# Kernel tuning notes

Measured on AMD Instinct MI355X. Metric: run time of the kernel, lower is better.

Reference implementation:

```python
import jax, jax.numpy as jnp
import numpy as np

N_ENT = 100000
N_USR = 30000
N_TOT = N_ENT + N_USR
N_REL = 32
D = 64
E = 500000
INTER = 500000
N_LAYERS = 2
SLOPE = 0.01  # torch nn.LeakyReLU default negative slope


def _seg_softmax(logits, seg, n):
    # sparse softmax over rows (segments)
    m = jax.ops.segment_max(logits, seg, num_segments=n)
    ex = jnp.exp(logits - m[seg])
    den = jax.ops.segment_sum(ex, seg, num_segments=n)
    return ex / den[seg]


def setup_inputs() -> dict:
    key = jax.random.key(0)
    k = jax.random.split(key, 14)
    all_embed = jax.random.normal(k[0], (N_TOT, D), jnp.float32) * 0.1
    rel_embed = jax.random.normal(k[1], (N_REL, D), jnp.float32) * 0.1
    Wk_w = jax.random.normal(k[2], (D, 2 * D), jnp.float32) / np.sqrt(2 * D)
    Wk_b = jnp.zeros((D,), jnp.float32)
    Wa_w = jax.random.normal(k[3], (D, D), jnp.float32) / np.sqrt(D)
    Wb_w = jax.random.normal(k[4], (D, D), jnp.float32) / np.sqrt(D)
    # KG edge lists (head entity, tail entity, relation)
    h_list = jnp.sort(jax.random.randint(k[5], (E,), 0, N_ENT))
    t_list = jax.random.randint(k[6], (E,), 0, N_ENT)
    r_list = jax.random.randint(k[7], (E,), 0, N_REL)
    # bipartite interaction matrix A_in (symmetric, items rows first then users)
    u = jax.random.randint(k[8], (INTER,), 0, N_USR)
    it = jax.random.randint(k[9], (INTER,), 0, N_ENT)
    a_row = jnp.concatenate([it, N_ENT + u])
    a_col = jnp.concatenate([N_ENT + u, it])
    a_vals = jax.random.uniform(k[10], (2 * INTER,), jnp.float32) * 0.01
    # calc_score ids: user ids are offset by n_entities in the concatenated table
    user_ids = N_ENT + jax.random.randint(k[11], (1024,), 0, N_USR)
    item_ids = jax.random.randint(k[12], (2048,), 0, N_ENT)
    return dict(all_embed=all_embed, rel_embed=rel_embed, Wk_w=Wk_w, Wk_b=Wk_b,
                Wa_w=Wa_w, Wb_w=Wb_w, a_vals=a_vals, user_ids=user_ids,
                item_ids=item_ids, h_list=h_list, t_list=t_list, r_list=r_list,
                a_row=a_row, a_col=a_col)


def _get_embeddings(all_embed, rel_embed, Wk_w, Wk_b, Wa_w, Wb_w, a_vals,
                    h_list, t_list, r_list, a_row, a_col):
    e_ent = all_embed[:N_ENT]
    e_usr = all_embed[N_ENT:]
    user_list = [e_usr]
    item_list = [e_ent]
    e_items_dual = e_ent
    e_users_curr = e_usr
    e_ent_curr = e_ent
    r_e = rel_embed[r_list]  # (E, D) -- constant across layers
    for _ in range(N_LAYERS):
        # --- KG attention (Eq. 2): gather + concat + linear + dot + leakyrelu ---
        h_e = e_ent_curr[h_list]            # (E, D)
        t_e = e_ent_curr[t_list]            # (E, D)
        cat = jnp.concatenate([t_e, h_e], axis=1)   # (E, 2D)
        trans = cat @ Wk_w.T + Wk_b                 # (E, D)
        logits = jnp.sum(trans * r_e, axis=1)       # (E,)
        vals = jnp.where(logits >= 0, logits, SLOPE * logits)
        alpha = _seg_softmax(vals, h_list, N_ENT)   # row-wise sparse softmax
        # --- KG aggregation (Eq. 1): spmm ---
        e_items_kg = jax.ops.segment_sum(alpha[:, None] * t_e, h_list,
                                         num_segments=N_ENT)
        # --- IG aggregation (Eq. 3 & 6): spmm with A_in ---
        ig_in = jnp.concatenate([e_items_dual, e_users_curr], axis=0)  # (N_TOT, D)
        ig_out = jax.ops.segment_sum(a_vals[:, None] * ig_in[a_col], a_row,
                                     num_segments=N_TOT)
        e_items_collab = ig_out[:N_ENT]
        e_users_new = ig_out[N_ENT:]
        # --- fusion gate (Eq. 4, 5) ---
        g = jax.nn.sigmoid(e_items_kg @ Wa_w.T + e_items_collab @ Wb_w.T)
        e_items_dual = g * e_items_kg + (1.0 - g) * e_items_collab
        item_list.append(e_items_collab)
        user_list.append(e_users_new)
        e_users_curr = e_users_new
        e_ent_curr = e_items_kg
    item_final = sum(item_list)
    user_final = sum(user_list)
    return jnp.concatenate([item_final, user_final], axis=0)


def reference(all_embed, rel_embed, Wk_w, Wk_b, Wa_w, Wb_w, a_vals,
              user_ids, item_ids, h_list, t_list, r_list, a_row, a_col):
    all_final = _get_embeddings(all_embed, rel_embed, Wk_w, Wk_b, Wa_w, Wb_w,
                                a_vals, h_list, t_list, r_list, a_row, a_col)
    user_e = all_final[user_ids]   # (Bu, D)
    item_e = all_final[item_ids]   # (Bi, D)
    return user_e @ item_e.T       # (Bu, Bi)
```

## Files before the change

### kernel.cpp

```cpp
#include <hip/hip_runtime.h>

#define N_ENT 100000
#define N_USR 30000
#define N_TOTN 130000
#define N_RELC 32
#define DIM 64
#define NEDGE 500000
#define INTER 500000
#define SLOPE 0.01f
#define CPT_NB 127
#define FILL_NB 489
#define MARK_NB 489
#define ATT_NB 512
#define SP_NB 512
#define RSTR 64
#define KGOFF_NB 1954

typedef unsigned char u8;
typedef unsigned long long u64;

__device__ __forceinline__ float grp_sum16(float v){
  v += __shfl_xor(v, 8, 64);
  v += __shfl_xor(v, 4, 64);
  v += __shfl_xor(v, 2, 64);
  v += __shfl_xor(v, 1, 64);
  return v;
}

__global__ void __launch_bounds__(256) k_prep(
    const float* __restrict__ rel, const float* __restrict__ Wk,
    const float* __restrict__ Wkb, float* __restrict__ m, float* __restrict__ b,
    const int* __restrict__ user_ids, const int* __restrict__ item_ids,
    u8* __restrict__ r2_item, u8* __restrict__ r2_user,
    const int* __restrict__ h_list, int* __restrict__ off){
  int bid = blockIdx.x;
  if (bid < 17){
    int idx = bid*256 + threadIdx.x;
    if (idx < N_RELC*128){
      int r = idx >> 7, j = idx & 127;
      float s = 0.f;
      for (int d = 0; d < DIM; ++d) s += rel[r*DIM+d] * Wk[d*128+j];
      m[idx] = s;
    } else if (idx < N_RELC*128 + N_RELC){
      int r = idx - N_RELC*128;
      float s = 0.f;
      for (int d = 0; d < DIM; ++d) s += Wkb[d] * rel[r*DIM+d];
      b[r] = s;
    }
  } else if (bid < 29){
    int i = (bid - 17)*256 + threadIdx.x;
    if (i < 1024) r2_user[user_ids[i] - N_ENT] = 1;
    else if (i < 3072) r2_item[item_ids[i - 1024]] = 1;
  } else {
    int e = (bid - 29)*256 + threadIdx.x;
    if (e <= NEDGE){
      int hc = (e < NEDGE) ? h_list[e] : N_ENT;
      int hp = (e == 0) ? -1 : h_list[e-1];
      for (int s = hp+1; s <= hc; ++s) off[s] = e;
    }
  }
}

__global__ void k_mark(const int4* __restrict__ a_row4, const int4* __restrict__ a_col4,
                       const u8* __restrict__ r2_item, const u8* __restrict__ r2_user,
                       u8* __restrict__ need_d, u8* __restrict__ need_u){
  int i = blockIdx.x*256 + threadIdx.x;
  if (i >= INTER/4) return;
  int4 ar = a_row4[i];
  int4 ac = a_col4[i];
  #pragma unroll
  for (int k = 0; k < 4; ++k){
    int it = (&ar.x)[k];
    int uu = (&ac.x)[k] - N_ENT;
    if (r2_item[it]) need_u[uu] = 1;
    if (r2_user[uu]) need_d[it] = 1;
  }
}

__global__ void __launch_bounds__(256) k_buildfill(
    const int* __restrict__ a_row, const int* __restrict__ a_col,
    const float* __restrict__ a_vals,
    const u8* __restrict__ need_d, const u8* __restrict__ need_u,
    const u8* __restrict__ r2_item, const u8* __restrict__ r2_user,
    int* __restrict__ list_gate, int* __restrict__ list_s1,
    int* __restrict__ counters, int* __restrict__ cnt, int2* __restrict__ csr){
  if (blockIdx.x < CPT_NB){
    __shared__ u64 mg_sh[16], ms_sh[16];
    __shared__ int pre_g[16], pre_s[16];
    __shared__ int base_sh[2];
    int t = threadIdx.x;
    int wave = t >> 6, lane = t & 63;
    bool pg[4], ps[4];
    int ibase = blockIdx.x*1024;
    #pragma unroll
    for (int k = 0; k < 4; ++k){
      int i = ibase + k*256 + t;
      bool g = false, s = false;
      if (i < N_TOTN){
        if (i < N_ENT){ g = need_d[i] != 0; s = (!g) && (r2_item[i] != 0); }
        else { int u = i - N_ENT; s = (need_u[u] != 0) || (r2_user[u] != 0); }
      }
      pg[k] = g; ps[k] = s;
      u64 mg = __ballot(g), ms = __ballot(s);
      if (lane == 0){ mg_sh[k*4 + wave] = mg; ms_sh[k*4 + wave] = ms; }
    }
    __syncthreads();
    if (t == 0){
      int sg = 0, ss = 0;
      for (int j = 0; j < 16; ++j){
        pre_g[j] = sg; sg += __popcll(mg_sh[j]);
        pre_s[j] = ss; ss += __popcll(ms_sh[j]);
      }
      base_sh[0] = sg ? atomicAdd(&counters[0], sg) : 0;
      base_sh[1] = ss ? atomicAdd(&counters[1], ss) : 0;
    }
    __syncthreads();
    int bg = base_sh[0], bs = base_sh[1];
    u64 lmask = (1ull << lane) - 1;
    #pragma unroll
    for (int k = 0; k < 4; ++k){
      int i = ibase + k*256 + t;
      if (pg[k]) list_gate[bg + pre_g[k*4+wave] + __popcll(mg_sh[k*4+wave] & lmask)] = i;
      if (ps[k]) list_s1 [bs + pre_s[k*4+wave] + __popcll(ms_sh[k*4+wave] & lmask)] = i;
    }
  } else {
    int i = (blockIdx.x - CPT_NB)*256 + threadIdx.x;
    if (i >= INTER/4) return;
    int4 ar = ((const int4*)a_row)[i];
    int4 ac = ((const int4*)a_col)[i];
    float4 av0 = ((const float4*)a_vals)[i];
    float4 av1 = ((const float4*)(a_vals + INTER))[i];
    #pragma unroll
    for (int k = 0; k < 4; ++k){
      int it = (&ar.x)[k];
      int uc = (&ac.x)[k];
      int uu = uc - N_ENT;
      if (need_d[it] | r2_item[it]){
        int p = atomicAdd(&cnt[it], 1);
        if (p < RSTR) csr[((size_t)it << 6) + p] = make_int2(uc, __float_as_int((&av0.x)[k]));
      }
      if (need_u[uu] | r2_user[uu]){
        int p = atomicAdd(&cnt[uc], 1);
        if (p < RSTR) csr[((size_t)uc << 6) + p] = make_int2(it, __float_as_int((&av1.x)[k]));
      }
    }
  }
}

__global__ void __launch_bounds__(512, 8) k_l1g(const float4* __restrict__ ent4,
    const float4* __restrict__ m4, const float* __restrict__ bvec,
    const float* __restrict__ Wa, const float* __restrict__ Wb,
    const int* __restrict__ off, const int* __restrict__ t_list,
    const int* __restrict__ r_list, const int* __restrict__ list_gate,
    const int* __restrict__ list_s1, const int* __restrict__ counters,
    const int* __restrict__ cnt, const int2* __restrict__ csr,
    float4* __restrict__ collab4, float4* __restrict__ x2_4){
  __shared__ float WaT[64][65];
  __shared__ float WbT[64][65];
  int t = threadIdx.x;
  if (blockIdx.x < ATT_NB){
    for (int i = t; i < 64*64; i += 512){
      int d = i >> 6, k = i & 63;
      WaT[k][d] = Wa[i];
      WbT[k][d] = Wb[i];
    }
    __syncthreads();
    int n = counters[0];
    int sub = t & 15;
    int grp = (blockIdx.x*512 + t) >> 4;
    int ng = (ATT_NB*512) >> 4;
    for (int idx = grp; idx < n; idx += ng){
      int s = list_gate[idx];
      int beg = off[s], end = off[s+1];
      float4 h4 = ent4[(size_t)s*16 + sub];
      float l = 0.f;
      float4 acc = {0.f,0.f,0.f,0.f};
      for (int base = beg; base < end; base += 16){
        int mch = end - base; if (mch > 16) mch = 16;
        int tj = 0, rj = 0;
        if (sub < mch){ tj = t_list[base + sub]; rj = r_list[base + sub]; }
        #pragma unroll 4
        for (int j = 0; j < mch; ++j){
          int ti = __shfl(tj, j, 16);
          int r  = __shfl(rj, j, 16);
          float4 t4 = ent4[(size_t)ti*16 + sub];
          float4 mt = m4[r*32 + sub];
          float4 mh = m4[r*32 + 16 + sub];
          float v = t4.x*mt.x + t4.y*mt.y + t4.z*mt.z + t4.w*mt.w
                  + h4.x*mh.x + h4.y*mh.y + h4.z*mh.z + h4.w*mh.w;
          v = grp_sum16(v) + bvec[r];
          v = (v >= 0.f) ? v : SLOPE * v;
          float w = __expf(v);
          l += w;
          acc.x += w*t4.x; acc.y += w*t4.y; acc.z += w*t4.z; acc.w += w*t4.w;
        }
      }
      float inv = (end > beg) ? 1.f / l : 0.f;
      float4 kg = {acc.x*inv, acc.y*inv, acc.z*inv, acc.w*inv};
      int deg = cnt[s]; if (deg > RSTR) deg = RSTR;
      size_t base0 = (size_t)s << 6;
      float4 cb = {0.f,0.f,0.f,0.f};
      for (int b = 0; b < deg; b += 16){
        int mch = deg - b; if (mch > 16) mch = 16;
        int2 e = make_int2(0, 0);
        if (sub < mch) e = csr[base0 + b + sub];
        #pragma unroll 4
        for (int j = 0; j < mch; ++j){
          int cj = __shfl(e.x, j, 16);
          float vj = __int_as_float(__shfl(e.y, j, 16));
          float4 sv = ent4[(size_t)cj*16 + sub];
          cb.x += vj*sv.x; cb.y += vj*sv.y; cb.z += vj*sv.z; cb.w += vj*sv.w;
        }
      }
      int d0 = sub*4;
      float4 ga = {0.f,0.f,0.f,0.f};
      for (int kk = 0; kk < 16; ++kk){
        float kqx = __shfl(kg.x, kk, 16), kqy = __shfl(kg.y, kk, 16);
        float kqz = __shfl(kg.z, kk, 16), kqw = __shfl(kg.w, kk, 16);
        float cqx = __shfl(cb.x, kk, 16), cqy = __shfl(cb.y, kk, 16);
        float cqz = __shfl(cb.z, kk, 16), cqw = __shfl(cb.w, kk, 16);
        int k0 = kk*4;
        #pragma unroll
        for (int j = 0; j < 4; ++j){
          float tsum = kqx*WaT[k0][d0+j] + kqy*WaT[k0+1][d0+j]
                     + kqz*WaT[k0+2][d0+j] + kqw*WaT[k0+3][d0+j]
                     + cqx*WbT[k0][d0+j] + cqy*WbT[k0+1][d0+j]
                     + cqz*WbT[k0+2][d0+j] + cqw*WbT[k0+3][d0+j];
          (&ga.x)[j] += tsum;
        }
      }
      float4 o;
      #pragma unroll
      for (int j = 0; j < 4; ++j){
        float g = 1.f / (1.f + __expf(-(&ga.x)[j]));
        (&o.x)[j] = g*(&kg.x)[j] + (1.f - g)*(&cb.x)[j];
      }
      collab4[(size_t)s*16 + sub] = cb;
      x2_4[(size_t)s*16 + sub] = o;
    }
  } else {
    int n = counters[1];
    int sub = t & 15;
    int bid = blockIdx.x - ATT_NB;
    int nb = gridDim.x - ATT_NB;
    int grp = (bid*512 + t) >> 4;
    int ng = (nb*512) >> 4;
    for (int idx = grp; idx < n; idx += ng){
      int i = list_s1[idx];
      int deg = cnt[i]; if (deg > RSTR) deg = RSTR;
      size_t base0 = (size_t)i << 6;
      float4 acc = {0.f,0.f,0.f,0.f};
      for (int b = 0; b < deg; b += 16){
        int mch = deg - b; if (mch > 16) mch = 16;
        int2 e = make_int2(0, 0);
        if (sub < mch) e = csr[base0 + b + sub];
        #pragma unroll 4
        for (int j = 0; j < mch; ++j){
          int cj = __shfl(e.x, j, 16);
          float vj = __int_as_float(__shfl(e.y, j, 16));
          float4 sv = ent4[(size_t)cj*16 + sub];
          acc.x += vj*sv.x; acc.y += vj*sv.y; acc.z += vj*sv.z; acc.w += vj*sv.w;
        }
      }
      if (i < N_ENT) collab4[(size_t)i*16 + sub] = acc;
      else x2_4[(size_t)i*16 + sub] = acc;
    }
  }
}

__global__ void __launch_bounds__(256) k_spmm2g(const int* __restrict__ cnt,
    const int2* __restrict__ csr, const float* __restrict__ x2,
    const float* __restrict__ all_embed, const float* __restrict__ collab1,
    const int* __restrict__ user_ids, const int* __restrict__ item_ids,
    float* __restrict__ user_e, float* __restrict__ item_e){
  int lane = threadIdx.x & 63;
  int g = (blockIdx.x*256 + threadIdx.x) >> 6;
  if (g >= 3072) return;
  int id;
  float b1;
  if (g < 1024){
    id = user_ids[g];
    b1 = x2[(size_t)id*64 + lane];
  } else {
    id = item_ids[g - 1024];
    b1 = collab1[(size_t)id*64 + lane];
  }
  float acc = all_embed[(size_t)id*64 + lane] + b1;
  int deg = cnt[id]; if (deg > RSTR) deg = RSTR;
  size_t base0 = (size_t)id << 6;
  int2 e = make_int2(0, 0);
  if (lane < deg) e = csr[base0 + lane];
  #pragma unroll 4
  for (int j = 0; j < deg; ++j){
    int cj = __shfl(e.x, j, 64);
    float vj = __int_as_float(__shfl(e.y, j, 64));
    acc += vj * x2[(size_t)cj*64 + lane];
  }
  if (g < 1024) user_e[(size_t)g*64 + lane] = acc;
  else item_e[(size_t)(g - 1024)*64 + lane] = acc;
}

__global__ void __launch_bounds__(256) k_out(const float* __restrict__ ue,
    const float* __restrict__ ie, float* __restrict__ out){
  __shared__ float ash[64][65];
  __shared__ float bsh[64][65];
  int row0 = blockIdx.y * 64, col0 = blockIdx.x * 64;
  for (int i = threadIdx.x; i < 64*64; i += 256){
    int r = i >> 6, c = i & 63;
    ash[r][c] = ue[(size_t)(row0 + r)*DIM + c];
    bsh[r][c] = ie[(size_t)(col0 + r)*DIM + c];
  }
  __syncthreads();
  int tx = threadIdx.x & 15, ty = threadIdx.x >> 4;
  int r0 = ty*4, c0 = tx*4;
  float acc[4][4] = {};
  #pragma unroll
  for (int k = 0; k < 64; ++k){
    float a0 = ash[r0][k], a1 = ash[r0+1][k], a2 = ash[r0+2][k], a3 = ash[r0+3][k];
    float b0 = bsh[c0][k], b1 = bsh[c0+1][k], b2 = bsh[c0+2][k], b3 = bsh[c0+3][k];
    acc[0][0] += a0*b0; acc[0][1] += a0*b1; acc[0][2] += a0*b2; acc[0][3] += a0*b3;
    acc[1][0] += a1*b0; acc[1][1] += a1*b1; acc[1][2] += a1*b2; acc[1][3] += a1*b3;
    acc[2][0] += a2*b0; acc[2][1] += a2*b1; acc[2][2] += a2*b2; acc[2][3] += a2*b3;
    acc[3][0] += a3*b0; acc[3][1] += a3*b1; acc[3][2] += a3*b2; acc[3][3] += a3*b3;
  }
  #pragma unroll
  for (int i = 0; i < 4; ++i){
    float4 o = {acc[i][0], acc[i][1], acc[i][2], acc[i][3]};
    *(float4*)&out[(size_t)(row0 + r0 + i)*2048 + col0 + c0] = o;
  }
}

extern "C" void kernel_launch(void* const* d_in, const int* in_sizes, int n_in,
                              void* d_out, int out_size, void* d_ws, size_t ws_size,
                              hipStream_t stream){
  const float* all_embed = (const float*)d_in[0];
  const float* rel_embed = (const float*)d_in[1];
  const float* Wk_w      = (const float*)d_in[2];
  const float* Wk_b      = (const float*)d_in[3];
  const float* Wa_w      = (const float*)d_in[4];
  const float* Wb_w      = (const float*)d_in[5];
  const float* a_vals    = (const float*)d_in[6];
  const int* user_ids   = (const int*)d_in[7];
  const int* item_ids   = (const int*)d_in[8];
  const int* h_list     = (const int*)d_in[9];
  const int* t_list     = (const int*)d_in[10];
  const int* r_list     = (const int*)d_in[11];
  const int* a_row      = (const int*)d_in[12];
  const int* a_col      = (const int*)d_in[13];
  float* out = (float*)d_out;

  char* p = (char*)d_ws;
  auto alloc = [&](size_t bytes)->void*{
    void* r = (void*)p;
    p += (bytes + 255) & ~(size_t)255;
    return r;
  };
  float* m_rel   = (float*)alloc((size_t)N_RELC*128*4);
  float* b_rel   = (float*)alloc((size_t)N_RELC*4);
  int*   kg_off  = (int*)  alloc((size_t)(N_ENT+1)*4);
  size_t zbytes = (size_t)N_TOTN*4 + 256 + (2*(size_t)N_ENT + 2*(size_t)N_USR);
  char*  zbase  = (char*)alloc(zbytes);
  int*   cnt      = (int*)zbase;
  int*   counters = (int*)(zbase + (size_t)N_TOTN*4);
  u8*    r2_item  = (u8*)(zbase + (size_t)N_TOTN*4 + 256);
  u8*    r2_user  = r2_item + N_ENT;
  u8*    need_d   = r2_user + N_USR;
  u8*    need_u   = need_d + N_ENT;
  int2*  csr     = (int2*) alloc((size_t)N_TOTN*RSTR*8);
  int*   list_gate = (int*)alloc((size_t)N_ENT*4);
  int*   list_s1   = (int*)alloc((size_t)N_TOTN*4);
  float* collab1 = (float*)alloc((size_t)N_ENT*DIM*4);
  float* x2      = (float*)alloc((size_t)N_TOTN*DIM*4);
  float* user_e  = (float*)alloc((size_t)1024*DIM*4);
  float* item_e  = (float*)alloc((size_t)2048*DIM*4);

  hipMemsetAsync(zbase, 0, zbytes, stream);
  k_prep<<<29 + KGOFF_NB, 256, 0, stream>>>(rel_embed, Wk_w, Wk_b,
      m_rel, b_rel, user_ids, item_ids, r2_item, r2_user, h_list, kg_off);
  k_mark<<<MARK_NB, 256, 0, stream>>>((const int4*)a_row, (const int4*)a_col,
      r2_item, r2_user, need_d, need_u);
  k_buildfill<<<CPT_NB + FILL_NB, 256, 0, stream>>>(a_row, a_col, a_vals,
      need_d, need_u, r2_item, r2_user, list_gate, list_s1, counters, cnt, csr);

  k_l1g<<<ATT_NB + SP_NB, 512, 0, stream>>>((const float4*)all_embed,
      (const float4*)m_rel, b_rel, Wa_w, Wb_w, kg_off, t_list, r_list,
      list_gate, list_s1, counters, cnt, csr, (float4*)collab1, (float4*)x2);

  k_spmm2g<<<768, 256, 0, stream>>>(cnt, csr, x2, all_embed, collab1,
      user_ids, item_ids, user_e, item_e);
  dim3 grid_out(2048/64, 1024/64);
  k_out<<<grid_out, 256, 0, stream>>>(user_e, item_e, out);
}
```

Measured before the change: 185.0 us.

## Fuse marking into front kernel with LDS bitmaps and drop gate LDS staging

Merges the mark kernel into the prep kernel. Each marking block rebuilds user/item bitmaps in shared memory, so the byte flags written by other blocks in the same launch are no longer needed there. Wa/Wb are pre-transposed once into global buffers, and the gate kernel reads them as float4 from cache instead of staging padded copies in LDS, which allows 256-thread blocks with twice as many blocks. It also raises unroll factors in the spmm loops. The cost is every marking block redoing a 3072-entry bitmap build, about 16KB of LDS per block, and more global loads in the gate loop.

New measurement: 188.8 us. 2.1% more time.

```diff
diff --git a/kernel.cpp b/kernel.cpp
--- a/kernel.cpp
+++ b/kernel.cpp
@@ -11,12 +11,18 @@
 #define CPT_NB 127
 #define FILL_NB 489
 #define MARK_NB 489
-#define ATT_NB 512
-#define SP_NB 512
+#define ATT_NB 1024
+#define SP_NB 1024
 #define RSTR 64
 #define KGOFF_NB 1954
+#define FR_TR 17
+#define FR_R2 19
+#define FR_KG 31
+#define FR_MK 1985
+#define FR_NB 2474
 
 typedef unsigned char u8;
+typedef unsigned int u32;
 typedef unsigned long long u64;
 
 __device__ __forceinline__ float grp_sum16(float v){
@@ -27,15 +33,20 @@
   return v;
 }
 
-__global__ void __launch_bounds__(256) k_prep(
+__global__ void __launch_bounds__(256) k_front(
     const float* __restrict__ rel, const float* __restrict__ Wk,
     const float* __restrict__ Wkb, float* __restrict__ m, float* __restrict__ b,
+    const float* __restrict__ Wa, const float* __restrict__ Wb,
+    float* __restrict__ wat, float* __restrict__ wbt,
     const int* __restrict__ user_ids, const int* __restrict__ item_ids,
     u8* __restrict__ r2_item, u8* __restrict__ r2_user,
-    const int* __restrict__ h_list, int* __restrict__ off){
+    const int* __restrict__ h_list, int* __restrict__ off,
+    const int4* __restrict__ a_row4, const int4* __restrict__ a_col4,
+    u8* __restrict__ need_d, u8* __restrict__ need_u){
   int bid = blockIdx.x;
-  if (bid < 17){
-    int idx = bid*256 + threadIdx.x;
+  int t = threadIdx.x;
+  if (bid < FR_TR){
+    int idx = bid*256 + t;
     if (idx < N_RELC*128){
       int r = idx >> 7, j = idx & 127;
       float s = 0.f;
@@ -47,33 +58,48 @@
       for (int d = 0; d < DIM; ++d) s += Wkb[d] * rel[r*DIM+d];
       b[r] = s;
     }
-  } else if (bid < 29){
-    int i = (bid - 17)*256 + threadIdx.x;
+  } else if (bid < FR_R2){
+    int base = (bid - FR_TR)*2048;
+    for (int i = t; i < 2048; i += 256){
+      int idx = base + i;
+      int k = idx >> 6, d = idx & 63;
+      wat[idx] = Wa[d*64 + k];
+      wbt[idx] = Wb[d*64 + k];
+    }
+  } else if (bid < FR_KG){
+    int i = (bid - FR_R2)*256 + t;
     if (i < 1024) r2_user[user_ids[i] - N_ENT] = 1;
     else if (i < 3072) r2_item[item_ids[i - 1024]] = 1;
-  } else {
-    int e = (bid - 29)*256 + threadIdx.x;
+  } else if (bid < FR_MK){
+    int e = (bid - FR_KG)*256 + t;
     if (e <= NEDGE){
       int hc = (e < NEDGE) ? h_list[e] : N_ENT;
       int hp = (e == 0) ? -1 : h_list[e-1];
       for (int s = hp+1; s <= hc; ++s) off[s] = e;
     }
-  }
-}
-
-__global__ void k_mark(const int4* __restrict__ a_row4, const int4* __restrict__ a_col4,
-                       const u8* __restrict__ r2_item, const u8* __restrict__ r2_user,
-                       u8* __restrict__ need_d, u8* __restrict__ need_u){
-  int i = blockIdx.x*256 + threadIdx.x;
-  if (i >= INTER/4) return;
-  int4 ar = a_row4[i];
-  int4 ac = a_col4[i];
-  #pragma unroll
-  for (int k = 0; k < 4; ++k){
-    int it = (&ar.x)[k];
-    int uu = (&ac.x)[k] - N_ENT;
-    if (r2_item[it]) need_u[uu] = 1;
-    if (r2_user[uu]) need_d[it] = 1;
+  } else {
+    __shared__ u32 bm_item[(N_ENT + 31)/32];
+    __shared__ u32 bm_user[(N_USR + 31)/32];
+    for (int i = t; i < (N_ENT+31)/32; i += 256) bm_item[i] = 0;
+    for (int i = t; i < (N_USR+31)/32; i += 256) bm_user[i] = 0;
+    __syncthreads();
+    for (int i = t; i < 3072; i += 256){
+      if (i < 1024){ int u = user_ids[i] - N_ENT; atomicOr(&bm_user[u>>5], 1u << (u&31)); }
+      else { int it = item_ids[i - 1024]; atomicOr(&bm_item[it>>5], 1u << (it&31)); }
+    }
+    __syncthreads();
+    int i = (bid - FR_MK)*256 + t;
+    if (i < INTER/4){
+      int4 ar = a_row4[i];
+      int4 ac = a_col4[i];
+      #pragma unroll
+      for (int k = 0; k < 4; ++k){
+        int it = (&ar.x)[k];
+        int uu = (&ac.x)[k] - N_ENT;
+        if ((bm_item[it>>5] >> (it&31)) & 1u) need_u[uu] = 1;
+        if ((bm_user[uu>>5] >> (uu&31)) & 1u) need_d[it] = 1;
+      }
+    }
   }
 }
 
@@ -147,28 +173,20 @@
   }
 }
 
-__global__ void __launch_bounds__(512, 8) k_l1g(const float4* __restrict__ ent4,
+__global__ void __launch_bounds__(256, 8) k_l1g(const float4* __restrict__ ent4,
     const float4* __restrict__ m4, const float* __restrict__ bvec,
-    const float* __restrict__ Wa, const float* __restrict__ Wb,
+    const float4* __restrict__ wat4, const float4* __restrict__ wbt4,
     const int* __restrict__ off, const int* __restrict__ t_list,
     const int* __restrict__ r_list, const int* __restrict__ list_gate,
     const int* __restrict__ list_s1, const int* __restrict__ counters,
     const int* __restrict__ cnt, const int2* __restrict__ csr,
     float4* __restrict__ collab4, float4* __restrict__ x2_4){
-  __shared__ float WaT[64][65];
-  __shared__ float WbT[64][65];
   int t = threadIdx.x;
+  int sub = t & 15;
   if (blockIdx.x < ATT_NB){
-    for (int i = t; i < 64*64; i += 512){
-      int d = i >> 6, k = i & 63;
-      WaT[k][d] = Wa[i];
-      WbT[k][d] = Wb[i];
-    }
-    __syncthreads();
     int n = counters[0];
-    int sub = t & 15;
-    int grp = (blockIdx.x*512 + t) >> 4;
-    int ng = (ATT_NB*512) >> 4;
+    int grp = (blockIdx.x*256 + t) >> 4;
+    int ng = (ATT_NB*256) >> 4;
     for (int idx = grp; idx < n; idx += ng){
       int s = list_gate[idx];
       int beg = off[s], end = off[s+1];
@@ -212,7 +230,6 @@
           cb.x += vj*sv.x; cb.y += vj*sv.y; cb.z += vj*sv.z; cb.w += vj*sv.w;
         }
       }
-      int d0 = sub*4;
       float4 ga = {0.f,0.f,0.f,0.f};
       for (int kk = 0; kk < 16; ++kk){
         float kqx = __shfl(kg.x, kk, 16), kqy = __shfl(kg.y, kk, 16);
@@ -220,14 +237,22 @@
         float cqx = __shfl(cb.x, kk, 16), cqy = __shfl(cb.y, kk, 16);
         float cqz = __shfl(cb.z, kk, 16), cqw = __shfl(cb.w, kk, 16);
         int k0 = kk*4;
-        #pragma unroll
-        for (int j = 0; j < 4; ++j){
-          float tsum = kqx*WaT[k0][d0+j] + kqy*WaT[k0+1][d0+j]
-                     + kqz*WaT[k0+2][d0+j] + kqw*WaT[k0+3][d0+j]
-                     + cqx*WbT[k0][d0+j] + cqy*WbT[k0+1][d0+j]
-                     + cqz*WbT[k0+2][d0+j] + cqw*WbT[k0+3][d0+j];
-          (&ga.x)[j] += tsum;
-        }
+        float4 wa0 = wat4[(k0+0)*16 + sub];
+        float4 wa1 = wat4[(k0+1)*16 + sub];
+        float4 wa2 = wat4[(k0+2)*16 + sub];
+        float4 wa3 = wat4[(k0+3)*16 + sub];
+        float4 wb0 = wbt4[(k0+0)*16 + sub];
+        float4 wb1 = wbt4[(k0+1)*16 + sub];
+        float4 wb2 = wbt4[(k0+2)*16 + sub];
+        float4 wb3 = wbt4[(k0+3)*16 + sub];
+        ga.x += kqx*wa0.x + kqy*wa1.x + kqz*wa2.x + kqw*wa3.x
+              + cqx*wb0.x + cqy*wb1.x + cqz*wb2.x + cqw*wb3.x;
+        ga.y += kqx*wa0.y + kqy*wa1.y + kqz*wa2.y + kqw*wa3.y
+              + cqx*wb0.y + cqy*wb1.y + cqz*wb2.y + cqw*wb3.y;
+        ga.z += kqx*wa0.z + kqy*wa1.z + kqz*wa2.z + kqw*wa3.z
+              + cqx*wb0.z + cqy*wb1.z + cqz*wb2.z + cqw*wb3.z;
+        ga.w += kqx*wa0.w + kqy*wa1.w + kqz*wa2.w + kqw*wa3.w
+              + cqx*wb0.w + cqy*wb1.w + cqz*wb2.w + cqw*wb3.w;
       }
       float4 o;
       #pragma unroll
@@ -240,11 +265,9 @@
     }
   } else {
     int n = counters[1];
-    int sub = t & 15;
     int bid = blockIdx.x - ATT_NB;
-    int nb = gridDim.x - ATT_NB;
-    int grp = (bid*512 + t) >> 4;
-    int ng = (nb*512) >> 4;
+    int grp = (bid*256 + t) >> 4;
+    int ng = (SP_NB*256) >> 4;
     for (int idx = grp; idx < n; idx += ng){
       int i = list_s1[idx];
       int deg = cnt[i]; if (deg > RSTR) deg = RSTR;
@@ -254,7 +277,7 @@
         int mch = deg - b; if (mch > 16) mch = 16;
         int2 e = make_int2(0, 0);
         if (sub < mch) e = csr[base0 + b + sub];
-        #pragma unroll 4
+        #pragma unroll 8
         for (int j = 0; j < mch; ++j){
           int cj = __shfl(e.x, j, 16);
           float vj = __int_as_float(__shfl(e.y, j, 16));
@@ -290,7 +313,7 @@
   size_t base0 = (size_t)id << 6;
   int2 e = make_int2(0, 0);
   if (lane < deg) e = csr[base0 + lane];
-  #pragma unroll 4
+  #pragma unroll 8
   for (int j = 0; j < deg; ++j){
     int cj = __shfl(e.x, j, 64);
     float vj = __int_as_float(__shfl(e.y, j, 64));
@@ -357,6 +380,8 @@
   };
   float* m_rel   = (float*)alloc((size_t)N_RELC*128*4);
   float* b_rel   = (float*)alloc((size_t)N_RELC*4);
+  float* wat     = (float*)alloc((size_t)64*64*4);
+  float* wbt     = (float*)alloc((size_t)64*64*4);
   int*   kg_off  = (int*)  alloc((size_t)(N_ENT+1)*4);
   size_t zbytes = (size_t)N_TOTN*4 + 256 + (2*(size_t)N_ENT + 2*(size_t)N_USR);
   char*  zbase  = (char*)alloc(zbytes);
@@ -375,16 +400,16 @@
   float* item_e  = (float*)alloc((size_t)2048*DIM*4);
 
   hipMemsetAsync(zbase, 0, zbytes, stream);
-  k_prep<<<29 + KGOFF_NB, 256, 0, stream>>>(rel_embed, Wk_w, Wk_b,
-      m_rel, b_rel, user_ids, item_ids, r2_item, r2_user, h_list, kg_off);
-  k_mark<<<MARK_NB, 256, 0, stream>>>((const int4*)a_row, (const int4*)a_col,
-      r2_item, r2_user, need_d, need_u);
+  k_front<<<FR_NB, 256, 0, stream>>>(rel_embed, Wk_w, Wk_b, m_rel, b_rel,
+      Wa_w, Wb_w, wat, wbt, user_ids, item_ids, r2_item, r2_user,
+      h_list, kg_off, (const int4*)a_row, (const int4*)a_col, need_d, need_u);
   k_buildfill<<<CPT_NB + FILL_NB, 256, 0, stream>>>(a_row, a_col, a_vals,
       need_d, need_u, r2_item, r2_user, list_gate, list_s1, counters, cnt, csr);
 
-  k_l1g<<<ATT_NB + SP_NB, 512, 0, stream>>>((const float4*)all_embed,
-      (const float4*)m_rel, b_rel, Wa_w, Wb_w, kg_off, t_list, r_list,
-      list_gate, list_s1, counters, cnt, csr, (float4*)collab1, (float4*)x2);
+  k_l1g<<<ATT_NB + SP_NB, 256, 0, stream>>>((const float4*)all_embed,
+      (const float4*)m_rel, b_rel, (const float4*)wat, (const float4*)wbt,
+      kg_off, t_list, r_list, list_gate, list_s1, counters, cnt, csr,
+      (float4*)collab1, (float4*)x2);
 
   k_spmm2g<<<768, 256, 0, stream>>>(cnt, csr, x2, all_embed, collab1,
       user_ids, item_ids, user_e, item_e);
```
